# Optimization experiments

Measured on AMD Instinct MI355X. Metric: run time of the kernel, lower is better.

## Reference

```python
import jax, jax.numpy as jnp
import numpy as np

EPS = 1e-8  # torch F.cosine_similarity eps


def setup_inputs() -> dict:
    key = jax.random.key(0)
    ks = jax.random.split(key, 10)
    S, B, V, D, H = 512, 128, 50257, 300, 512
    return {
        "context": jax.random.randint(ks[0], (32, B), 0, V),
        "ends": jax.random.randint(ks[1], (S, B), 0, V),
        "ends_ls": jax.random.randint(ks[2], (B,), 0, S),
        "embed_mat": jax.random.normal(ks[3], (V, D), jnp.float32),
        "w_ih": jax.random.normal(ks[4], (3 * H, 1), jnp.float32) * 0.05,
        "w_hh": jax.random.normal(ks[5], (3 * H, H), jnp.float32) * 0.05,
        "b_ih": jax.random.normal(ks[6], (3 * H,), jnp.float32) * 0.05,
        "b_hh": jax.random.normal(ks[7], (3 * H,), jnp.float32) * 0.05,
        "fc_w": jax.random.normal(ks[8], (1, H), jnp.float32) * 0.05,
        "fc_b": jax.random.normal(ks[9], (1,), jnp.float32) * 0.05,
    }


def _rep_features(embeds):
    # embeds: [S, B, D]. Causal max cosine similarity per position/batch.
    S = embeds.shape[0]
    norms = jnp.linalg.norm(embeds, axis=-1, keepdims=True)  # [S,B,1]
    xn = embeds / jnp.maximum(norms, EPS)
    sims = jnp.einsum("ibd,jbd->ijb", xn, xn)  # [S,S,B]
    sims = jnp.where(jnp.isnan(sims), -1.0, sims)  # sims[sims != sims] = -1
    i = jnp.arange(S)[:, None]
    j = jnp.arange(S)[None, :]
    causal = (j < i)[:, :, None]  # strictly past positions
    sims = jnp.where(causal, sims, -jnp.inf)
    feats = jnp.max(sims, axis=1)  # [S,B]
    feats = feats.at[0].set(0.0)  # position 0 -> zeros
    return feats


def _gru(x_seq, w_ih, w_hh, b_ih, b_hh, h0):
    # x_seq: [S, B, 1]; returns final hidden state [B, H]
    H = h0.shape[-1]

    def step(h, x):
        gi = x @ w_ih.T + b_ih  # [B, 3H]
        gh = h @ w_hh.T + b_hh
        ir, iz, inn = gi[:, :H], gi[:, H:2 * H], gi[:, 2 * H:]
        hr, hz, hn = gh[:, :H], gh[:, H:2 * H], gh[:, 2 * H:]
        r = jax.nn.sigmoid(ir + hr)
        z = jax.nn.sigmoid(iz + hz)
        n = jnp.tanh(inn + r * hn)
        h_new = (1.0 - z) * n + z * h
        return h_new, None

    h_last, _ = jax.lax.scan(step, h0, x_seq)
    return h_last


def reference(context, ends, ends_ls, embed_mat, w_ih, w_hh, b_ih, b_hh, fc_w, fc_b):
    S, B = ends.shape
    embeds = embed_mat[ends.reshape(-1)].reshape(S, B, -1)  # [S,B,D]
    feats = _rep_features(embeds)[:, :, None]  # [S,B,1]
    h0 = jnp.zeros((B, w_hh.shape[-1]), feats.dtype)
    h_last = _gru(feats, w_ih, w_hh, b_ih, b_hh, h0)  # [B,H]
    final = (h_last @ fc_w.T + fc_b).reshape(-1)  # [B]
    return final
```

## Files before the change

kernel.cpp:

```cpp
#include <hip/hip_runtime.h>
#include <hip/hip_bf16.h>
#include <math.h>

#define S_LEN 512
#define B_N   128
#define D_EMB 300
#define KP    320
#define H_N   512

typedef __attribute__((ext_vector_type(8)))  short short8;
typedef __attribute__((ext_vector_type(8)))  unsigned short ushort8;
typedef __attribute__((ext_vector_type(4)))  unsigned int uint4v;
typedef __attribute__((ext_vector_type(4)))  float float4v;
typedef __attribute__((ext_vector_type(16))) float float16v;

__device__ __forceinline__ unsigned short f32_to_bf16(float f) {
  unsigned u = __float_as_uint(f);
  u = (u + 0x7fffu + ((u >> 16) & 1u)) >> 16;
  return (unsigned short)u;
}
__device__ __forceinline__ float bf16_to_f32(unsigned short h) {
  return __uint_as_float(((unsigned)h) << 16);
}
__device__ __forceinline__ short8 as_short8(uint4v v) {
  union { uint4v u; short8 s; } c; c.u = v; return c.s;
}

__global__ __launch_bounds__(256) void k1_embed_norm(
    const int* __restrict__ ends, const float* __restrict__ emb,
    unsigned short* __restrict__ xh, unsigned short* __restrict__ xl) {
  int wave = threadIdx.x >> 6, lane = threadIdx.x & 63;
  int vec = blockIdx.x * 4 + wave;
  int b = vec & (B_N - 1), s = vec >> 7;
  int v = ends[vec];
  const float* row = emb + (size_t)v * D_EMB;
  float e0 = row[lane], e1 = row[lane + 64], e2 = row[lane + 128], e3 = row[lane + 192];
  float e4 = (lane + 256 < D_EMB) ? row[lane + 256] : 0.f;
  float ss = e0*e0 + e1*e1 + e2*e2 + e3*e3 + e4*e4;
  #pragma unroll
  for (int m = 1; m < 64; m <<= 1) ss += __shfl_xor(ss, m);
  float sc = 1.0f / fmaxf(sqrtf(ss), 1e-8f);
  size_t base = ((size_t)b * S_LEN + s) * KP;
  float xs[5] = { e0*sc, e1*sc, e2*sc, e3*sc, (lane + 256 < D_EMB) ? e4*sc : 0.f };
  #pragma unroll
  for (int i = 0; i < 5; ++i) {
    unsigned short hi = f32_to_bf16(xs[i]);
    unsigned short lo = f32_to_bf16(xs[i] - bf16_to_f32(hi));
    xh[base + lane + 64*i] = hi;
    xl[base + lane + 64*i] = lo;
  }
}

#define KC  80
#define LDP 88

__global__ __launch_bounds__(256) void k2_feats(
    const unsigned short* __restrict__ xh, const unsigned short* __restrict__ xl,
    float* __restrict__ feats) {
  __shared__ __align__(16) unsigned short sBh[64*LDP], sBl[64*LDP];
  __shared__ float rbuf[4][32];
  int b   = blockIdx.x;
  int ic  = blockIdx.y;
  int tid = threadIdx.x;
  int wave = tid >> 6, lane = tid & 63;
  int itl = wave & 1, jtl = wave >> 1;
  int itg = ic * 2 + itl;
  size_t xbase = (size_t)b * S_LEN * KP;
  int arow0 = ic * 64;
  const size_t arowoff = xbase + (size_t)(arow0 + itl * 32 + (lane & 31)) * KP
                       + (size_t)((lane >> 5) * 8);

  float rm[16];
  #pragma unroll
  for (int r = 0; r < 16; ++r) rm[r] = -INFINITY;

  for (int jc = 0; jc <= ic; ++jc) {
    int jt = jc * 2 + jtl;
    bool active = (jt <= itg);
    float16v acc;
    #pragma unroll
    for (int r = 0; r < 16; ++r) acc[r] = 0.f;

    for (int kc = 0; kc < 4; ++kc) {
      short8 a_h[5], a_l[5];
      #pragma unroll
      for (int ks = 0; ks < 5; ++ks) {
        size_t ga = arowoff + kc * KC + ks * 16;
        a_h[ks] = *(const short8*)&xh[ga];
        a_l[ks] = *(const short8*)&xl[ga];
      }
      __syncthreads();
      for (int u = tid; u < 640; u += 256) {
        int r = u / 10, sg = u % 10;
        size_t gb = xbase + (size_t)(jc*64 + r) * KP + kc*KC + sg*8;
        int la = r * LDP + sg * 8;
        *(ushort8*)&sBh[la] = *(const ushort8*)&xh[gb];
        *(ushort8*)&sBl[la] = *(const ushort8*)&xl[gb];
      }
      __syncthreads();
      if (active) {
        int br = (jtl*32 + (lane & 31)) * LDP;
        int kq = (lane >> 5) * 8;
        #pragma unroll
        for (int ks = 0; ks < 5; ++ks) {
          short8 b_h = *(const short8*)&sBh[br + ks*16 + kq];
          short8 b_l = *(const short8*)&sBl[br + ks*16 + kq];
          acc = __builtin_amdgcn_mfma_f32_32x32x16_bf16(a_h[ks], b_h, acc, 0, 0, 0);
          acc = __builtin_amdgcn_mfma_f32_32x32x16_bf16(a_h[ks], b_l, acc, 0, 0, 0);
          acc = __builtin_amdgcn_mfma_f32_32x32x16_bf16(a_l[ks], b_h, acc, 0, 0, 0);
        }
      }
    }
    if (active) {
      int colg = jt * 32 + (lane & 31);
      #pragma unroll
      for (int r = 0; r < 16; ++r) {
        int rowg = itg * 32 + (r & 3) + 8*(r >> 2) + 4*(lane >> 5);
        float v = acc[r];
        if (jt == itg && colg >= rowg) v = -INFINITY;
        rm[r] = fmaxf(rm[r], v);
      }
    }
  }
  #pragma unroll
  for (int r = 0; r < 16; ++r) {
    float v = rm[r];
    v = fmaxf(v, __shfl_xor(v, 1));
    v = fmaxf(v, __shfl_xor(v, 2));
    v = fmaxf(v, __shfl_xor(v, 4));
    v = fmaxf(v, __shfl_xor(v, 8));
    v = fmaxf(v, __shfl_xor(v, 16));
    rm[r] = v;
  }
  if ((lane & 31) == 0) {
    int half = lane >> 5;
    #pragma unroll
    for (int r = 0; r < 16; ++r)
      rbuf[wave][(r & 3) + 8*(r >> 2) + 4*half] = rm[r];
  }
  __syncthreads();
  if (tid < 64) {
    int it2 = tid >> 5, rl = tid & 31;
    float v = fmaxf(rbuf[it2][rl], rbuf[it2 + 2][rl]);
    int i = ic * 64 + it2 * 32 + rl;
    feats[i * B_N + b] = (i == 0) ? 0.0f : v;
  }
}

#define HW64 (B_N * H_N / 2)

__global__ __launch_bounds__(256, 1) void k3_gru(
    const float* __restrict__ feats,
    const float* __restrict__ w_ih, const float* __restrict__ w_hh,
    const float* __restrict__ b_ih, const float* __restrict__ b_hh,
    const float* __restrict__ fc_w, const float* __restrict__ fc_b,
    unsigned long long* __restrict__ hq, unsigned int* __restrict__ bars,
    float* __restrict__ out) {
  __shared__ __align__(16) float4v red2[4][16][16];
  __shared__ float osum[256];
  int tid = threadIdx.x;
  int wave = tid >> 6, lane = tid & 63;
  int g = blockIdx.x & 7, s = blockIdx.x >> 3;

  short8 wfh[3][4], wfl[3][4];
  {
    int nloc = lane & 15;
    int kq = (lane >> 4) * 8;
    #pragma unroll
    for (int gt = 0; gt < 3; ++gt) {
      const float* wr = w_hh + (size_t)(gt * H_N + s * 16 + nloc) * H_N;
      #pragma unroll
      for (int ks = 0; ks < 4; ++ks) {
        int k0 = wave * 128 + ks * 32 + kq;
        short8 h8, l8;
        #pragma unroll
        for (int j = 0; j < 8; ++j) {
          float wv = wr[k0 + j];
          unsigned short hi = f32_to_bf16(wv);
          unsigned short lo = f32_to_bf16(wv - bf16_to_f32(hi));
          h8[j] = (short)hi; l8[j] = (short)lo;
        }
        wfh[gt][ks] = h8; wfl[gt][ks] = l8;
      }
    }
  }
  int bb = tid >> 4, jj = tid & 15;
  int jr = s * 16 + jj;
  float wihr = w_ih[jr], wihz = w_ih[H_N + jr], wihn = w_ih[2*H_N + jr];
  float bir = b_ih[jr],  biz = b_ih[H_N + jr],  bin_ = b_ih[2*H_N + jr];
  float bhr = b_hh[jr],  bhz = b_hh[H_N + jr],  bhn = b_hh[2*H_N + jr];
  float fcw = fc_w[jr];
  int gb = g * 16 + bb;
  float h_old = 0.f;
  const unsigned int* fp = bars + g * 32 + wave * 8 + (lane & 7);
  unsigned int* myflag = bars + g * 32 + s;

  const int Cp = g * 16 + (s >> 3) * 4 + ((s >> 1) & 3);
  const int qp = (2 * s + (jj >> 3)) & 3;
  const size_t prodoff = (size_t)Cp * 512 + (size_t)qp * 128 + (size_t)bb * 8;
  const size_t cbase = (size_t)(g * 16 + wave * 4) * 512 + (size_t)lane * 8;

  for (int t = 0; t < S_LEN; ++t) {
    float x = feats[t * B_N + gb];
    float sr = 0.f, sz = 0.f, sn = 0.f;
    if (t > 0) {
      {
        const unsigned tgt = (unsigned)t;
        for (;;) {
          unsigned f = __hip_atomic_load(fp, __ATOMIC_RELAXED, __HIP_MEMORY_SCOPE_AGENT);
          if (__ballot(f < tgt) == 0ull) break;
          __builtin_amdgcn_s_sleep(1);
        }
        asm volatile("" ::: "memory");
      }
      const unsigned short* hh =
          (const unsigned short*)(hq + (size_t)((t - 1) & 1) * HW64);
      const unsigned short* hbase = hh + cbase;
      const unsigned short* lbase = hbase + 65536;
      uint4v rh0, rh1, rh2, rh3, rl0, rl1, rl2, rl3;
      asm volatile(
        "global_load_dwordx4 %0, %8, off sc1\n\t"
        "global_load_dwordx4 %1, %8, off offset:1024 sc1\n\t"
        "global_load_dwordx4 %2, %8, off offset:2048 sc1\n\t"
        "global_load_dwordx4 %3, %8, off offset:3072 sc1\n\t"
        "global_load_dwordx4 %4, %9, off sc1\n\t"
        "global_load_dwordx4 %5, %9, off offset:1024 sc1\n\t"
        "global_load_dwordx4 %6, %9, off offset:2048 sc1\n\t"
        "global_load_dwordx4 %7, %9, off offset:3072 sc1\n\t"
        "s_waitcnt vmcnt(0)"
        : "=&v"(rh0), "=&v"(rh1), "=&v"(rh2), "=&v"(rh3),
          "=&v"(rl0), "=&v"(rl1), "=&v"(rl2), "=&v"(rl3)
        : "v"(hbase), "v"(lbase)
        : "memory");
      short8 ah[4] = { as_short8(rh0), as_short8(rh1), as_short8(rh2), as_short8(rh3) };
      short8 al[4] = { as_short8(rl0), as_short8(rl1), as_short8(rl2), as_short8(rl3) };
      float4v a0, a1, a2;
      #pragma unroll
      for (int r = 0; r < 4; ++r) { a0[r] = 0.f; a1[r] = 0.f; a2[r] = 0.f; }
      #pragma unroll
      for (int ks = 0; ks < 4; ++ks) {
        a0 = __builtin_amdgcn_mfma_f32_16x16x32_bf16(ah[ks], wfh[0][ks], a0, 0,0,0);
        a1 = __builtin_amdgcn_mfma_f32_16x16x32_bf16(ah[ks], wfh[1][ks], a1, 0,0,0);
        a2 = __builtin_amdgcn_mfma_f32_16x16x32_bf16(ah[ks], wfh[2][ks], a2, 0,0,0);
        a0 = __builtin_amdgcn_mfma_f32_16x16x32_bf16(ah[ks], wfl[0][ks], a0, 0,0,0);
        a1 = __builtin_amdgcn_mfma_f32_16x16x32_bf16(ah[ks], wfl[1][ks], a1, 0,0,0);
        a2 = __builtin_amdgcn_mfma_f32_16x16x32_bf16(ah[ks], wfl[2][ks], a2, 0,0,0);
        a0 = __builtin_amdgcn_mfma_f32_16x16x32_bf16(al[ks], wfh[0][ks], a0, 0,0,0);
        a1 = __builtin_amdgcn_mfma_f32_16x16x32_bf16(al[ks], wfh[1][ks], a1, 0,0,0);
        a2 = __builtin_amdgcn_mfma_f32_16x16x32_bf16(al[ks], wfh[2][ks], a2, 0,0,0);
      }
      int colw = lane & 15, roww = (lane >> 4) * 4;
      #pragma unroll
      for (int r = 0; r < 4; ++r) {
        float4v w; w[0] = a0[r]; w[1] = a1[r]; w[2] = a2[r]; w[3] = 0.f;
        red2[wave][roww + r][colw] = w;
      }
      __syncthreads();
      float4v s0 = red2[0][bb][jj], s1 = red2[1][bb][jj];
      float4v s2 = red2[2][bb][jj], s3 = red2[3][bb][jj];
      sr = s0[0] + s1[0] + s2[0] + s3[0];
      sz = s0[1] + s1[1] + s2[1] + s3[1];
      sn = s0[2] + s1[2] + s2[2] + s3[2];
    }
    float ar_ = fminf(fmaxf(x * wihr + bir + sr + bhr, -30.f), 30.f);
    float az_ = fminf(fmaxf(x * wihz + biz + sz + bhz, -30.f), 30.f);
    float r_ = __builtin_amdgcn_rcpf(1.f + __expf(-ar_));
    float z_ = __builtin_amdgcn_rcpf(1.f + __expf(-az_));
    float an_ = fminf(fmaxf(x * wihn + bin_ + r_ * (sn + bhn), -30.f), 30.f);
    float en = __expf(-2.f * an_);
    float n_ = (1.f - en) * __builtin_amdgcn_rcpf(1.f + en);
    float h_new = (1.f - z_) * n_ + z_ * h_old;
    h_old = h_new;
    if (t < S_LEN - 1) {
      unsigned short hi16 = f32_to_bf16(h_new);
      unsigned short lo16 = f32_to_bf16(h_new - bf16_to_f32(hi16));
      unsigned myh = hi16, myl = lo16;
      unsigned oh = (unsigned)__shfl_xor((int)myh, 1);
      unsigned ol = (unsigned)__shfl_xor((int)myl, 1);
      bool od1 = (jj & 1) != 0;
      unsigned pH = od1 ? (oh | (myh << 16)) : (myh | (oh << 16));
      unsigned pL = od1 ? (ol | (myl << 16)) : (myl | (ol << 16));
      unsigned qh = (unsigned)__shfl_xor((int)pH, 2);
      unsigned ql = (unsigned)__shfl_xor((int)pL, 2);
      bool od2 = (jj & 2) != 0;
      unsigned h01 = od2 ? qh : pH, h23 = od2 ? pH : qh;
      unsigned l01 = od2 ? ql : pL, l23 = od2 ? pL : ql;
      unsigned xh01 = (unsigned)__shfl_xor((int)h01, 4);
      unsigned xh23 = (unsigned)__shfl_xor((int)h23, 4);
      unsigned xl01 = (unsigned)__shfl_xor((int)l01, 4);
      unsigned xl23 = (unsigned)__shfl_xor((int)l23, 4);
      bool od4 = (jj & 4) != 0;
      uint4v runH, runL;
      runH[0] = od4 ? xh01 : h01; runH[1] = od4 ? xh23 : h23;
      runH[2] = od4 ? h01 : xh01; runH[3] = od4 ? h23 : xh23;
      runL[0] = od4 ? xl01 : l01; runL[1] = od4 ? xl23 : l23;
      runL[2] = od4 ? l01 : xl01; runL[3] = od4 ? l23 : xl23;
      unsigned short* hh = (unsigned short*)(hq + (size_t)(t & 1) * HW64);
      if ((jj & 3) == 0) {
        if ((jj & 4) == 0) *(uint4v*)(hh + prodoff)         = runH;
        else               *(uint4v*)(hh + 65536 + prodoff) = runL;
      }
      asm volatile("s_waitcnt vmcnt(0)" ::: "memory");
      __syncthreads();
      if (tid == 0)
        __hip_atomic_store(myflag, (unsigned)(t + 1),
                           __ATOMIC_RELAXED, __HIP_MEMORY_SCOPE_WORKGROUP);
    }
  }
  osum[tid] = h_old * fcw;
  __syncthreads();
  if (jj == 0) {
    float acc = 0.f;
    #pragma unroll
    for (int q = 0; q < 16; ++q) acc += osum[bb * 16 + q];
    if (s == 0) acc += fc_b[0];
    atomicAdd(&out[gb], acc);
  }
}

extern "C" void kernel_launch(void* const* d_in, const int* in_sizes, int n_in,
                              void* d_out, int out_size, void* d_ws, size_t ws_size,
                              hipStream_t stream) {
  (void)in_sizes; (void)n_in; (void)out_size; (void)ws_size;
  const int*   ends = (const int*)d_in[1];
  const float* emb  = (const float*)d_in[3];
  const float* w_ih = (const float*)d_in[4];
  const float* w_hh = (const float*)d_in[5];
  const float* b_ih = (const float*)d_in[6];
  const float* b_hh = (const float*)d_in[7];
  const float* fc_w = (const float*)d_in[8];
  const float* fc_b = (const float*)d_in[9];
  float* out = (float*)d_out;

  size_t xn_elems = (size_t)B_N * S_LEN * KP;
  unsigned short* xh = (unsigned short*)d_ws;
  unsigned short* xl = xh + xn_elems;
  float* feats = (float*)(xl + xn_elems);
  unsigned long long* hq = (unsigned long long*)(feats + S_LEN * B_N);
  unsigned int* bars = (unsigned int*)(hq + 2 * (size_t)HW64);

  hipMemsetAsync(out, 0, sizeof(float) * B_N, stream);
  hipMemsetAsync(bars, 0, 4096, stream);

  k1_embed_norm<<<dim3(S_LEN * B_N / 4), dim3(256), 0, stream>>>(ends, emb, xh, xl);
  k2_feats<<<dim3(B_N, 8), dim3(256), 0, stream>>>(xh, xl, feats);

  void* args[] = { (void*)&feats, (void*)&w_ih, (void*)&w_hh, (void*)&b_ih,
                   (void*)&b_hh, (void*)&fc_w, (void*)&fc_b,
                   (void*)&hq, (void*)&bars, (void*)&out };
  hipLaunchCooperativeKernel((void*)k3_gru, dim3(256), dim3(256), args, 0, stream);
}
```

Before: 1.108 ms.

## Split GRU recurrent matmul K-dimension across 8 waves per block

```diff
diff --git a/kernel.cpp b/kernel.cpp
--- a/kernel.cpp
+++ b/kernel.cpp
@@ -149,20 +149,20 @@
 
 #define HW64 (B_N * H_N / 2)
 
-__global__ __launch_bounds__(256, 1) void k3_gru(
+__global__ __launch_bounds__(512, 1) void k3_gru(
     const float* __restrict__ feats,
     const float* __restrict__ w_ih, const float* __restrict__ w_hh,
     const float* __restrict__ b_ih, const float* __restrict__ b_hh,
     const float* __restrict__ fc_w, const float* __restrict__ fc_b,
     unsigned long long* __restrict__ hq, unsigned int* __restrict__ bars,
     float* __restrict__ out) {
-  __shared__ __align__(16) float4v red2[4][16][16];
+  __shared__ __align__(16) float4v red2[8][16][16];
   __shared__ float osum[256];
   int tid = threadIdx.x;
   int wave = tid >> 6, lane = tid & 63;
   int g = blockIdx.x & 7, s = blockIdx.x >> 3;
 
-  short8 wfh[3][4], wfl[3][4];
+  short8 wfh[3][2], wfl[3][2];
   {
     int nloc = lane & 15;
     int kq = (lane >> 4) * 8;
@@ -170,8 +170,8 @@
     for (int gt = 0; gt < 3; ++gt) {
       const float* wr = w_hh + (size_t)(gt * H_N + s * 16 + nloc) * H_N;
       #pragma unroll
-      for (int ks = 0; ks < 4; ++ks) {
-        int k0 = wave * 128 + ks * 32 + kq;
+      for (int ks = 0; ks < 2; ++ks) {
+        int k0 = wave * 64 + ks * 32 + kq;
         short8 h8, l8;
         #pragma unroll
         for (int j = 0; j < 8; ++j) {
@@ -184,24 +184,25 @@
       }
     }
   }
+  const bool gater = (tid < 256);
   int bb = tid >> 4, jj = tid & 15;
   int jr = s * 16 + jj;
   float wihr = w_ih[jr], wihz = w_ih[H_N + jr], wihn = w_ih[2*H_N + jr];
   float bir = b_ih[jr],  biz = b_ih[H_N + jr],  bin_ = b_ih[2*H_N + jr];
   float bhr = b_hh[jr],  bhz = b_hh[H_N + jr],  bhn = b_hh[2*H_N + jr];
   float fcw = fc_w[jr];
-  int gb = g * 16 + bb;
+  int gb = g * 16 + (bb & 15);
   float h_old = 0.f;
-  const unsigned int* fp = bars + g * 32 + wave * 8 + (lane & 7);
+  const unsigned int* fp = bars + g * 32 + wave * 4 + (lane & 3);
   unsigned int* myflag = bars + g * 32 + s;
 
   const int Cp = g * 16 + (s >> 3) * 4 + ((s >> 1) & 3);
   const int qp = (2 * s + (jj >> 3)) & 3;
-  const size_t prodoff = (size_t)Cp * 512 + (size_t)qp * 128 + (size_t)bb * 8;
-  const size_t cbase = (size_t)(g * 16 + wave * 4) * 512 + (size_t)lane * 8;
+  const size_t prodoff = (size_t)Cp * 512 + (size_t)qp * 128 + (size_t)(bb & 15) * 8;
+  const size_t cbase = (size_t)(g * 16 + wave * 2) * 512 + (size_t)lane * 8;
 
   for (int t = 0; t < S_LEN; ++t) {
-    float x = feats[t * B_N + gb];
+    float x = gater ? feats[t * B_N + gb] : 0.f;
     float sr = 0.f, sz = 0.f, sn = 0.f;
     if (t > 0) {
       {
@@ -217,38 +218,39 @@
           (const unsigned short*)(hq + (size_t)((t - 1) & 1) * HW64);
       const unsigned short* hbase = hh + cbase;
       const unsigned short* lbase = hbase + 65536;
-      uint4v rh0, rh1, rh2, rh3, rl0, rl1, rl2, rl3;
+      uint4v rh0, rh1, rl0, rl1;
       asm volatile(
-        "global_load_dwordx4 %0, %8, off sc1\n\t"
-        "global_load_dwordx4 %1, %8, off offset:1024 sc1\n\t"
-        "global_load_dwordx4 %2, %8, off offset:2048 sc1\n\t"
-        "global_load_dwordx4 %3, %8, off offset:3072 sc1\n\t"
-        "global_load_dwordx4 %4, %9, off sc1\n\t"
-        "global_load_dwordx4 %5, %9, off offset:1024 sc1\n\t"
-        "global_load_dwordx4 %6, %9, off offset:2048 sc1\n\t"
-        "global_load_dwordx4 %7, %9, off offset:3072 sc1\n\t"
+        "global_load_dwordx4 %0, %4, off sc1\n\t"
+        "global_load_dwordx4 %1, %4, off offset:1024 sc1\n\t"
+        "global_load_dwordx4 %2, %5, off sc1\n\t"
+        "global_load_dwordx4 %3, %5, off offset:1024 sc1\n\t"
         "s_waitcnt vmcnt(0)"
-        : "=&v"(rh0), "=&v"(rh1), "=&v"(rh2), "=&v"(rh3),
-          "=&v"(rl0), "=&v"(rl1), "=&v"(rl2), "=&v"(rl3)
+        : "=&v"(rh0), "=&v"(rh1), "=&v"(rl0), "=&v"(rl1)
         : "v"(hbase), "v"(lbase)
         : "memory");
-      short8 ah[4] = { as_short8(rh0), as_short8(rh1), as_short8(rh2), as_short8(rh3) };
-      short8 al[4] = { as_short8(rl0), as_short8(rl1), as_short8(rl2), as_short8(rl3) };
+      short8 ah0 = as_short8(rh0), ah1 = as_short8(rh1);
+      short8 al0 = as_short8(rl0), al1 = as_short8(rl1);
       float4v a0, a1, a2;
       #pragma unroll
       for (int r = 0; r < 4; ++r) { a0[r] = 0.f; a1[r] = 0.f; a2[r] = 0.f; }
-      #pragma unroll
-      for (int ks = 0; ks < 4; ++ks) {
-        a0 = __builtin_amdgcn_mfma_f32_16x16x32_bf16(ah[ks], wfh[0][ks], a0, 0,0,0);
-        a1 = __builtin_amdgcn_mfma_f32_16x16x32_bf16(ah[ks], wfh[1][ks], a1, 0,0,0);
-        a2 = __builtin_amdgcn_mfma_f32_16x16x32_bf16(ah[ks], wfh[2][ks], a2, 0,0,0);
-        a0 = __builtin_amdgcn_mfma_f32_16x16x32_bf16(ah[ks], wfl[0][ks], a0, 0,0,0);
-        a1 = __builtin_amdgcn_mfma_f32_16x16x32_bf16(ah[ks], wfl[1][ks], a1, 0,0,0);
-        a2 = __builtin_amdgcn_mfma_f32_16x16x32_bf16(ah[ks], wfl[2][ks], a2, 0,0,0);
-        a0 = __builtin_amdgcn_mfma_f32_16x16x32_bf16(al[ks], wfh[0][ks], a0, 0,0,0);
-        a1 = __builtin_amdgcn_mfma_f32_16x16x32_bf16(al[ks], wfh[1][ks], a1, 0,0,0);
-        a2 = __builtin_amdgcn_mfma_f32_16x16x32_bf16(al[ks], wfh[2][ks], a2, 0,0,0);
-      }
+      a0 = __builtin_amdgcn_mfma_f32_16x16x32_bf16(ah0, wfh[0][0], a0, 0,0,0);
+      a1 = __builtin_amdgcn_mfma_f32_16x16x32_bf16(ah0, wfh[1][0], a1, 0,0,0);
+      a2 = __builtin_amdgcn_mfma_f32_16x16x32_bf16(ah0, wfh[2][0], a2, 0,0,0);
+      a0 = __builtin_amdgcn_mfma_f32_16x16x32_bf16(ah0, wfl[0][0], a0, 0,0,0);
+      a1 = __builtin_amdgcn_mfma_f32_16x16x32_bf16(ah0, wfl[1][0], a1, 0,0,0);
+      a2 = __builtin_amdgcn_mfma_f32_16x16x32_bf16(ah0, wfl[2][0], a2, 0,0,0);
+      a0 = __builtin_amdgcn_mfma_f32_16x16x32_bf16(al0, wfh[0][0], a0, 0,0,0);
+      a1 = __builtin_amdgcn_mfma_f32_16x16x32_bf16(al0, wfh[1][0], a1, 0,0,0);
+      a2 = __builtin_amdgcn_mfma_f32_16x16x32_bf16(al0, wfh[2][0], a2, 0,0,0);
+      a0 = __builtin_amdgcn_mfma_f32_16x16x32_bf16(ah1, wfh[0][1], a0, 0,0,0);
+      a1 = __builtin_amdgcn_mfma_f32_16x16x32_bf16(ah1, wfh[1][1], a1, 0,0,0);
+      a2 = __builtin_amdgcn_mfma_f32_16x16x32_bf16(ah1, wfh[2][1], a2, 0,0,0);
+      a0 = __builtin_amdgcn_mfma_f32_16x16x32_bf16(ah1, wfl[0][1], a0, 0,0,0);
+      a1 = __builtin_amdgcn_mfma_f32_16x16x32_bf16(ah1, wfl[1][1], a1, 0,0,0);
+      a2 = __builtin_amdgcn_mfma_f32_16x16x32_bf16(ah1, wfl[2][1], a2, 0,0,0);
+      a0 = __builtin_amdgcn_mfma_f32_16x16x32_bf16(al1, wfh[0][1], a0, 0,0,0);
+      a1 = __builtin_amdgcn_mfma_f32_16x16x32_bf16(al1, wfh[1][1], a1, 0,0,0);
+      a2 = __builtin_amdgcn_mfma_f32_16x16x32_bf16(al1, wfh[2][1], a2, 0,0,0);
       int colw = lane & 15, roww = (lane >> 4) * 4;
       #pragma unroll
       for (int r = 0; r < 4; ++r) {
@@ -256,50 +258,55 @@
         red2[wave][roww + r][colw] = w;
       }
       __syncthreads();
-      float4v s0 = red2[0][bb][jj], s1 = red2[1][bb][jj];
-      float4v s2 = red2[2][bb][jj], s3 = red2[3][bb][jj];
-      sr = s0[0] + s1[0] + s2[0] + s3[0];
-      sz = s0[1] + s1[1] + s2[1] + s3[1];
-      sn = s0[2] + s1[2] + s2[2] + s3[2];
-    }
-    float ar_ = fminf(fmaxf(x * wihr + bir + sr + bhr, -30.f), 30.f);
-    float az_ = fminf(fmaxf(x * wihz + biz + sz + bhz, -30.f), 30.f);
-    float r_ = __builtin_amdgcn_rcpf(1.f + __expf(-ar_));
-    float z_ = __builtin_amdgcn_rcpf(1.f + __expf(-az_));
-    float an_ = fminf(fmaxf(x * wihn + bin_ + r_ * (sn + bhn), -30.f), 30.f);
-    float en = __expf(-2.f * an_);
-    float n_ = (1.f - en) * __builtin_amdgcn_rcpf(1.f + en);
-    float h_new = (1.f - z_) * n_ + z_ * h_old;
-    h_old = h_new;
+      if (gater) {
+        float4v sv = red2[0][bb][jj];
+        #pragma unroll
+        for (int w8 = 1; w8 < 8; ++w8) sv += red2[w8][bb][jj];
+        sr = sv[0]; sz = sv[1]; sn = sv[2];
+      }
+    }
+    if (gater) {
+      float ar_ = fminf(fmaxf(x * wihr + bir + sr + bhr, -30.f), 30.f);
+      float az_ = fminf(fmaxf(x * wihz + biz + sz + bhz, -30.f), 30.f);
+      float r_ = __builtin_amdgcn_rcpf(1.f + __expf(-ar_));
+      float z_ = __builtin_amdgcn_rcpf(1.f + __expf(-az_));
+      float an_ = fminf(fmaxf(x * wihn + bin_ + r_ * (sn + bhn), -30.f), 30.f);
+      float en = __expf(-2.f * an_);
+      float n_ = (1.f - en) * __builtin_amdgcn_rcpf(1.f + en);
+      float h_new = (1.f - z_) * n_ + z_ * h_old;
+      h_old = h_new;
+      if (t < S_LEN - 1) {
+        unsigned short hi16 = f32_to_bf16(h_new);
+        unsigned short lo16 = f32_to_bf16(h_new - bf16_to_f32(hi16));
+        unsigned myh = hi16, myl = lo16;
+        unsigned oh = (unsigned)__shfl_xor((int)myh, 1);
+        unsigned ol = (unsigned)__shfl_xor((int)myl, 1);
+        bool od1 = (jj & 1) != 0;
+        unsigned pH = od1 ? (oh | (myh << 16)) : (myh | (oh << 16));
+        unsigned pL = od1 ? (ol | (myl << 16)) : (myl | (ol << 16));
+        unsigned qh = (unsigned)__shfl_xor((int)pH, 2);
+        unsigned ql = (unsigned)__shfl_xor((int)pL, 2);
+        bool od2 = (jj & 2) != 0;
+        unsigned h01 = od2 ? qh : pH, h23 = od2 ? pH : qh;
+        unsigned l01 = od2 ? ql : pL, l23 = od2 ? pL : ql;
+        unsigned xh01 = (unsigned)__shfl_xor((int)h01, 4);
+        unsigned xh23 = (unsigned)__shfl_xor((int)h23, 4);
+        unsigned xl01 = (unsigned)__shfl_xor((int)l01, 4);
+        unsigned xl23 = (unsigned)__shfl_xor((int)l23, 4);
+        bool od4 = (jj & 4) != 0;
+        uint4v runH, runL;
+        runH[0] = od4 ? xh01 : h01; runH[1] = od4 ? xh23 : h23;
+        runH[2] = od4 ? h01 : xh01; runH[3] = od4 ? h23 : xh23;
+        runL[0] = od4 ? xl01 : l01; runL[1] = od4 ? xl23 : l23;
+        runL[2] = od4 ? l01 : xl01; runL[3] = od4 ? l23 : xl23;
+        unsigned short* hh = (unsigned short*)(hq + (size_t)(t & 1) * HW64);
+        if ((jj & 3) == 0) {
+          if ((jj & 4) == 0) *(uint4v*)(hh + prodoff)         = runH;
+          else               *(uint4v*)(hh + 65536 + prodoff) = runL;
+        }
+      }
+    }
     if (t < S_LEN - 1) {
-      unsigned short hi16 = f32_to_bf16(h_new);
-      unsigned short lo16 = f32_to_bf16(h_new - bf16_to_f32(hi16));
-      unsigned myh = hi16, myl = lo16;
-      unsigned oh = (unsigned)__shfl_xor((int)myh, 1);
-      unsigned ol = (unsigned)__shfl_xor((int)myl, 1);
-      bool od1 = (jj & 1) != 0;
-      unsigned pH = od1 ? (oh | (myh << 16)) : (myh | (oh << 16));
-      unsigned pL = od1 ? (ol | (myl << 16)) : (myl | (ol << 16));
-      unsigned qh = (unsigned)__shfl_xor((int)pH, 2);
-      unsigned ql = (unsigned)__shfl_xor((int)pL, 2);
-      bool od2 = (jj & 2) != 0;
-      unsigned h01 = od2 ? qh : pH, h23 = od2 ? pH : qh;
-      unsigned l01 = od2 ? ql : pL, l23 = od2 ? pL : ql;
-      unsigned xh01 = (unsigned)__shfl_xor((int)h01, 4);
-      unsigned xh23 = (unsigned)__shfl_xor((int)h23, 4);
-      unsigned xl01 = (unsigned)__shfl_xor((int)l01, 4);
-      unsigned xl23 = (unsigned)__shfl_xor((int)l23, 4);
-      bool od4 = (jj & 4) != 0;
-      uint4v runH, runL;
-      runH[0] = od4 ? xh01 : h01; runH[1] = od4 ? xh23 : h23;
-      runH[2] = od4 ? h01 : xh01; runH[3] = od4 ? h23 : xh23;
-      runL[0] = od4 ? xl01 : l01; runL[1] = od4 ? xl23 : l23;
-      runL[2] = od4 ? l01 : xl01; runL[3] = od4 ? l23 : xl23;
-      unsigned short* hh = (unsigned short*)(hq + (size_t)(t & 1) * HW64);
-      if ((jj & 3) == 0) {
-        if ((jj & 4) == 0) *(uint4v*)(hh + prodoff)         = runH;
-        else               *(uint4v*)(hh + 65536 + prodoff) = runL;
-      }
       asm volatile("s_waitcnt vmcnt(0)" ::: "memory");
       __syncthreads();
       if (tid == 0)
@@ -307,9 +314,9 @@
                            __ATOMIC_RELAXED, __HIP_MEMORY_SCOPE_WORKGROUP);
     }
   }
-  osum[tid] = h_old * fcw;
+  if (gater) osum[tid] = h_old * fcw;
   __syncthreads();
-  if (jj == 0) {
+  if (gater && jj == 0) {
     float acc = 0.f;
     #pragma unroll
     for (int q = 0; q < 16; ++q) acc += osum[bb * 16 + q];
@@ -348,5 +355,5 @@
   void* args[] = { (void*)&feats, (void*)&w_ih, (void*)&w_hh, (void*)&b_ih,
                    (void*)&b_hh, (void*)&fc_w, (void*)&fc_b,
                    (void*)&hq, (void*)&bars, (void*)&out };
-  hipLaunchCooperativeKernel((void*)k3_gru, dim3(256), dim3(256), args, 0, stream);
-}
+  hipLaunchCooperativeKernel((void*)k3_gru, dim3(256), dim3(512), args, 0, stream);
+}
```

After: 1.093 ms. Within noise of the previous version (-1.4%).
